# Performance work log

Measured on AMD Instinct MI355X. Metric: run time of the kernel, lower is better.

Reference implementation:

```python
import jax, jax.numpy as jnp
import numpy as np

FEAT = 1024
B = 1024
S = 64


def setup_inputs() -> dict:
    key = jax.random.key(0)
    ks = jax.random.split(key, 6)
    scale_ih = 1.0 / np.sqrt(2 * FEAT)
    scale_hh = 1.0 / np.sqrt(FEAT)
    return {
        "query": jax.random.normal(ks[0], (B, FEAT), jnp.float32) * 0.1,
        "support_context": jax.random.normal(ks[1], (S, FEAT), jnp.float32) * 0.1,
        "W_ih": jax.random.normal(ks[2], (4 * FEAT, 2 * FEAT), jnp.float32) * scale_ih,
        "W_hh": jax.random.normal(ks[3], (4 * FEAT, FEAT), jnp.float32) * scale_hh,
        "b_ih": jax.random.normal(ks[4], (4 * FEAT,), jnp.float32) * scale_hh,
        "b_hh": jax.random.normal(ks[5], (4 * FEAT,), jnp.float32) * scale_hh,
    }


def reference(query, support_context, W_ih, W_hh, b_ih, b_hh):
    # query: [B, F]; support_context: [S, F]; steps == S
    hidden = query
    cell = jnp.zeros_like(query)
    support_t = support_context.T  # [F, S]

    def step(carry, _):
        h, c = carry
        attn = jax.nn.softmax(h @ support_t, axis=1)          # [B, S]
        readout = attn @ support_context                      # [B, F]
        x = jnp.concatenate([query, readout], axis=1)         # [B, 2F]
        gates = x @ W_ih.T + b_ih + h @ W_hh.T + b_hh          # [B, 4F]
        i, f, g, o = jnp.split(gates, 4, axis=1)               # torch LSTMCell gate order
        c_new = jax.nn.sigmoid(f) * c + jax.nn.sigmoid(i) * jnp.tanh(g)
        h_new = jax.nn.sigmoid(o) * jnp.tanh(c_new) + query   # skip connection per original
        return (h_new, c_new), None

    (hidden, cell), _ = jax.lax.scan(step, (hidden, cell), None,
                                     length=support_context.shape[0])
    return hidden
```

## Files before the change

### kernel.cpp

```cpp
#include <hip/hip_runtime.h>
#include <hip/hip_bf16.h>


typedef __attribute__((ext_vector_type(8))) __bf16 bf16x8;
typedef __attribute__((ext_vector_type(4))) float f32x4;
typedef __attribute__((ext_vector_type(8))) unsigned short ushort8;

__device__ __forceinline__ ushort f2bf(float f) {
  union { float f; unsigned int u; } v; v.f = f;
  unsigned int u = v.u;
  u += 0x7FFFu + ((u >> 16) & 1u);
  return (ushort)(u >> 16);
}
__device__ __forceinline__ float bf2f(ushort u) {
  union { float f; unsigned int u; } v; v.u = ((unsigned int)u) << 16; return v.f;
}
__device__ __forceinline__ float sigm_(float x) { return 1.f / (1.f + __expf(-x)); }
__device__ __forceinline__ float tanh_(float x) {
  x = fminf(15.f, fmaxf(-15.f, x));
  float e = __expf(2.f * x);
  return (e - 1.f) / (e + 1.f);
}
__device__ __forceinline__ void async16(ushort* lds, const ushort* g) {
  __builtin_amdgcn_global_load_lds(
      (const __attribute__((address_space(1))) void*)g,
      (__attribute__((address_space(3))) void*)lds, 16, 0, 0);
}
__device__ __forceinline__ int permrow(int n) {
  int g = n >> 10, j = n & 1023;
  return ((j >> 4) << 6) | (g << 4) | (j & 15);
}

__global__ __launch_bounds__(256) void prep_kernel(
    const float* __restrict__ query, const float* __restrict__ support,
    const float* __restrict__ W_ih, const float* __restrict__ W_hh,
    const float* __restrict__ b_ih, const float* __restrict__ b_hh,
    ushort* __restrict__ Wq_bf, ushort* __restrict__ Wcomb,
    float* __restrict__ bias_p, ushort* __restrict__ X0,
    float* __restrict__ c, ushort* __restrict__ Wr_bf,
    ushort* __restrict__ Sb)
{
  int g = blockIdx.x * 256 + threadIdx.x;
  int n = g >> 10, k = g & 1023;
  int np = permrow(n);
  Wq_bf[(size_t)np * 1024 + k] = f2bf(W_ih[(size_t)n * 2048 + k]);
  Wr_bf[(size_t)n * 1024 + k]  = f2bf(W_ih[(size_t)n * 2048 + 1024 + k]);
  Wcomb[(size_t)np * 1088 + k] = f2bf(W_hh[(size_t)n * 1024 + k]);
  if (g < 1024 * 1024) {
    X0[g] = f2bf(query[g]);
    c[g] = 0.f;
  }
  if (g < 4096) bias_p[permrow(g)] = b_ih[g] + b_hh[g];
  if (g < 65536) Sb[g] = f2bf(support[g]);
}

__global__ __launch_bounds__(256) void sw_mfma(
    const ushort* __restrict__ Wr, const ushort* __restrict__ Sb,
    ushort* __restrict__ Wcomb)
{
  __shared__ ushort As[3][128 * 32];
  __shared__ ushort Bs[3][64 * 32];
  const int t = threadIdx.x;
  const int bm0 = blockIdx.x * 128;
  const int w = t >> 6, l = t & 63;
  const int wm = w * 32;
  const int srow = t >> 2, scol = (t & 3) * 8;
  const ushort* ga0 = Wr + (size_t)(bm0 + srow) * 1024 + scol;
  const ushort* ga1 = Wr + (size_t)(bm0 + 64 + srow) * 1024 + scol;
  const ushort* gb0 = Sb + (size_t)srow * 1024 + scol;
  const int fr = l & 15, fk = (l >> 4) * 8, fq = l >> 4;
  f32x4 acc[2][4] = {};
  const int nt = 32;
  async16(&As[0][t * 8], ga0); async16(&As[0][2048 + t * 8], ga1);
  async16(&Bs[0][t * 8], gb0);
  async16(&As[1][t * 8], ga0 + 32); async16(&As[1][2048 + t * 8], ga1 + 32);
  async16(&Bs[1][t * 8], gb0 + 32);
  for (int it = 0; it < nt; it++) {
    if (it + 1 < nt) { asm volatile("s_waitcnt vmcnt(3)" ::: "memory"); }
    else             { asm volatile("s_waitcnt vmcnt(0)" ::: "memory"); }
    __builtin_amdgcn_s_barrier();
    __builtin_amdgcn_sched_barrier(0);
    const int b = it % 3;
    const ushort* pa = &As[b][(wm + fr) * 32 + fk];
    const ushort* pb = &Bs[b][fr * 32 + fk];
    bf16x8 af[2], bfv[4];
#pragma unroll
    for (int mi = 0; mi < 2; mi++) af[mi] = *(const bf16x8*)(pa + mi * 512);
#pragma unroll
    for (int ni = 0; ni < 4; ni++) bfv[ni] = *(const bf16x8*)(pb + ni * 512);
    if (it + 2 < nt) {
      const int pbuf = (it + 2) % 3;
      const int k0 = (it + 2) << 5;
      async16(&As[pbuf][t * 8], ga0 + k0); async16(&As[pbuf][2048 + t * 8], ga1 + k0);
      async16(&Bs[pbuf][t * 8], gb0 + k0);
    }
#pragma unroll
    for (int mi = 0; mi < 2; mi++)
#pragma unroll
      for (int ni = 0; ni < 4; ni++)
        acc[mi][ni] = __builtin_amdgcn_mfma_f32_16x16x32_bf16(af[mi], bfv[ni], acc[mi][ni], 0, 0, 0);
  }
#pragma unroll
  for (int mi = 0; mi < 2; mi++)
#pragma unroll
    for (int ni = 0; ni < 4; ni++) {
      int s = ni * 16 + fr;
      int row0 = bm0 + wm + mi * 16 + fq * 4;
#pragma unroll
      for (int jj = 0; jj < 4; jj++)
        Wcomb[(size_t)permrow(row0 + jj) * 1088 + 1024 + s] = f2bf(acc[mi][ni][jj]);
    }
}

__global__ __launch_bounds__(256) void gemm_base(
    const ushort* __restrict__ A, const ushort* __restrict__ Bw,
    const float* __restrict__ bias, float* __restrict__ Cout)
{
  __shared__ ushort As[3][2][64 * 32];
  __shared__ ushort Bs[3][2][128 * 32];
  const int t = threadIdx.x;
  const int bid = blockIdx.x;
  const int xcd = bid & 7, idx = bid >> 3;
  const int bx = idx & 15, byy = idx >> 4;
  const int by = xcd * 4 + byy;
  const int m0 = bx * 64, n0 = by * 128;
  const int w = t >> 6, l = t & 63;
  const int wm = (w >> 1) * 32, wn = (w & 1) * 64;
  const int srow = t >> 2, scol = (t & 3) * 8;
  const ushort* ga  = A  + (size_t)(m0 + srow) * 1024 + scol;
  const ushort* gb0 = Bw + (size_t)(n0 + srow) * 1024 + scol;
  const ushort* gb1 = Bw + (size_t)(n0 + 64 + srow) * 1024 + scol;
  const int fr = l & 15, fk = (l >> 4) * 8, fq = l >> 4;
  f32x4 acc[2][4] = {};
  const int nt = 16;
#define BSTAGE(buf, k0)                                       \
  async16(&As[buf][0][t * 8], ga + (k0));                     \
  async16(&As[buf][1][t * 8], ga + (k0) + 32);                \
  async16(&Bs[buf][0][t * 8], gb0 + (k0));                    \
  async16(&Bs[buf][0][2048 + t * 8], gb1 + (k0));             \
  async16(&Bs[buf][1][t * 8], gb0 + (k0) + 32);               \
  async16(&Bs[buf][1][2048 + t * 8], gb1 + (k0) + 32);
  BSTAGE(0, 0)
  BSTAGE(1, 64)
  for (int it = 0; it < nt; it++) {
    if (it + 1 < nt) { asm volatile("s_waitcnt vmcnt(6)" ::: "memory"); }
    else             { asm volatile("s_waitcnt vmcnt(0)" ::: "memory"); }
    __builtin_amdgcn_s_barrier();
    __builtin_amdgcn_sched_barrier(0);
    if (it + 2 < nt) { const int pb = (it + 2) % 3; const int k0 = (it + 2) << 6; BSTAGE(pb, k0) }
    const int b = it % 3;
#pragma unroll
    for (int kk = 0; kk < 2; kk++) {
      const ushort* pa = &As[b][kk][(wm + fr) * 32 + fk];
      const ushort* pb2 = &Bs[b][kk][(wn + fr) * 32 + fk];
      bf16x8 af[2], bfv[4];
#pragma unroll
      for (int mi = 0; mi < 2; mi++) af[mi] = *(const bf16x8*)(pa + mi * 512);
#pragma unroll
      for (int ni = 0; ni < 4; ni++) bfv[ni] = *(const bf16x8*)(pb2 + ni * 512);
      __builtin_amdgcn_s_setprio(1);
#pragma unroll
      for (int mi = 0; mi < 2; mi++)
#pragma unroll
        for (int ni = 0; ni < 4; ni++)
          acc[mi][ni] = __builtin_amdgcn_mfma_f32_16x16x32_bf16(af[mi], bfv[ni], acc[mi][ni], 0, 0, 0);
      __builtin_amdgcn_s_setprio(0);
    }
  }
#undef BSTAGE
#pragma unroll
  for (int mi = 0; mi < 2; mi++)
#pragma unroll
    for (int ni = 0; ni < 4; ni++) {
      int col = n0 + wn + ni * 16 + fr;
      int row0 = m0 + wm + mi * 16 + fq * 4;
      float bv = bias[col];
#pragma unroll
      for (int jj = 0; jj < 4; jj++)
        Cout[(size_t)(row0 + jj) * 4096 + col] = acc[mi][ni][jj] + bv;
    }
}

__global__ __launch_bounds__(256, 2) void gemm_fused(
    const ushort* __restrict__ A,
    const ushort* __restrict__ Wcomb,
    const ushort* __restrict__ Sb,
    const float* __restrict__ base,
    float* __restrict__ cbuf, const float* __restrict__ query,
    ushort* __restrict__ Xout, float* __restrict__ outp)
{
  __shared__ ushort As[3][2][64 * 32];
  __shared__ ushort Bs[3][2][128 * 32];
  const int t = threadIdx.x;
  const int bid = blockIdx.x;
  const int xcd = bid & 7, idx = bid >> 3;
  const int bx = idx & 15, byy = idx >> 4;
  const int by = xcd * 4 + byy;
  const int m0 = bx * 64, n0 = by * 128;
  const int w = t >> 6, l = t & 63;
  const int wm = (w >> 1) * 32, wn = (w & 1) * 64;
  const int srow = t >> 2, scol = (t & 3) * 8;
  const ushort* ga  = A + (size_t)(m0 + srow) * 1024 + scol;
  const ushort* gb0 = Wcomb + (size_t)(n0 + srow) * 1088 + scol;
  const ushort* gb1 = Wcomb + (size_t)(n0 + 64 + srow) * 1088 + scol;
  const int fr = l & 15, fk = (l >> 4) * 8, fq = l >> 4;
  const ushort* gsb = Sb + (size_t)((w & 1) * 32 + fr) * 1024 + fk;
  f32x4 acc[2][4] = {};
  f32x4 lacc[2][2] = {};
#define FSTAGE_A(buf, k0)                                     \
  async16(&As[buf][0][t * 8], ga + (k0));                     \
  async16(&As[buf][1][t * 8], ga + (k0) + 32);
#define FSTAGE_B(buf, k0)                                     \
  async16(&Bs[buf][0][t * 8], gb0 + (k0));                    \
  async16(&Bs[buf][0][2048 + t * 8], gb1 + (k0));             \
  async16(&Bs[buf][1][t * 8], gb0 + (k0) + 32);               \
  async16(&Bs[buf][1][2048 + t * 8], gb1 + (k0) + 32);
  FSTAGE_A(0, 0) FSTAGE_B(0, 0)
  FSTAGE_A(1, 64) FSTAGE_B(1, 64)
  asm volatile("s_waitcnt vmcnt(6)" ::: "memory");
  for (int it = 0; it < 16; it++) {
    __builtin_amdgcn_s_barrier();
    __builtin_amdgcn_sched_barrier(0);
    const int k0 = it << 6;
    bf16x8 sb00 = *(const bf16x8*)(gsb + k0);
    bf16x8 sb01 = *(const bf16x8*)(gsb + k0 + 32);
    bf16x8 sb10 = *(const bf16x8*)(gsb + k0 + 16384);
    bf16x8 sb11 = *(const bf16x8*)(gsb + k0 + 16384 + 32);
    if (it <= 13) { const int pb = (it + 2) % 3; FSTAGE_A(pb, k0 + 128) FSTAGE_B(pb, k0 + 128) }
    else if (it == 14) { FSTAGE_B(1, 1024) }
    const int b = it % 3;
    bf16x8 af2[2][2];
#pragma unroll
    for (int kk = 0; kk < 2; kk++) {
      const ushort* pa = &As[b][kk][(wm + fr) * 32 + fk];
      const ushort* pb2 = &Bs[b][kk][(wn + fr) * 32 + fk];
      bf16x8 bfv[4];
#pragma unroll
      for (int mi = 0; mi < 2; mi++) af2[kk][mi] = *(const bf16x8*)(pa + mi * 512);
#pragma unroll
      for (int ni = 0; ni < 4; ni++) bfv[ni] = *(const bf16x8*)(pb2 + ni * 512);
      __builtin_amdgcn_s_setprio(1);
#pragma unroll
      for (int mi = 0; mi < 2; mi++)
#pragma unroll
        for (int ni = 0; ni < 4; ni++)
          acc[mi][ni] = __builtin_amdgcn_mfma_f32_16x16x32_bf16(af2[kk][mi], bfv[ni], acc[mi][ni], 0, 0, 0);
      __builtin_amdgcn_s_setprio(0);
    }
    if (it <= 13)      { asm volatile("s_waitcnt vmcnt(6)" ::: "memory"); }
    else if (it == 14) { asm volatile("s_waitcnt vmcnt(4)" ::: "memory"); }
    else               { asm volatile("s_waitcnt vmcnt(0)" ::: "memory"); }
    __builtin_amdgcn_sched_barrier(0);
    lacc[0][0] = __builtin_amdgcn_mfma_f32_16x16x32_bf16(af2[0][0], sb00, lacc[0][0], 0, 0, 0);
    lacc[0][1] = __builtin_amdgcn_mfma_f32_16x16x32_bf16(af2[0][0], sb10, lacc[0][1], 0, 0, 0);
    lacc[1][0] = __builtin_amdgcn_mfma_f32_16x16x32_bf16(af2[0][1], sb00, lacc[1][0], 0, 0, 0);
    lacc[1][1] = __builtin_amdgcn_mfma_f32_16x16x32_bf16(af2[0][1], sb10, lacc[1][1], 0, 0, 0);
    lacc[0][0] = __builtin_amdgcn_mfma_f32_16x16x32_bf16(af2[1][0], sb01, lacc[0][0], 0, 0, 0);
    lacc[0][1] = __builtin_amdgcn_mfma_f32_16x16x32_bf16(af2[1][0], sb11, lacc[0][1], 0, 0, 0);
    lacc[1][0] = __builtin_amdgcn_mfma_f32_16x16x32_bf16(af2[1][1], sb01, lacc[1][0], 0, 0, 0);
    lacc[1][1] = __builtin_amdgcn_mfma_f32_16x16x32_bf16(af2[1][1], sb11, lacc[1][1], 0, 0, 0);
  }
  __builtin_amdgcn_s_barrier();
  {
    float* lg = (float*)&Bs[0][0][0];
    const int sbase = (w & 1) * 32;
#pragma unroll
    for (int mi = 0; mi < 2; mi++)
#pragma unroll
      for (int ni = 0; ni < 2; ni++) {
        int s = sbase + ni * 16 + fr;
        int r0 = wm + mi * 16 + fq * 4;
#pragma unroll
        for (int jj = 0; jj < 4; jj++)
          lg[(r0 + jj) * 64 + s] = lacc[mi][ni][jj];
      }
  }
  __syncthreads();
  {
    const int r = t >> 2, q = t & 3;
    float* lg = (float*)&Bs[0][0][0];
    float p[16];
#pragma unroll
    for (int i = 0; i < 16; i++) p[i] = lg[r * 64 + q * 16 + i];
    float mx = p[0];
#pragma unroll
    for (int i = 1; i < 16; i++) mx = fmaxf(mx, p[i]);
    mx = fmaxf(mx, __shfl_xor(mx, 1));
    mx = fmaxf(mx, __shfl_xor(mx, 2));
    float sm = 0.f;
#pragma unroll
    for (int i = 0; i < 16; i++) { p[i] = __expf(p[i] - mx); sm += p[i]; }
    sm += __shfl_xor(sm, 1);
    sm += __shfl_xor(sm, 2);
    float inv = 1.f / sm;
    ushort* at = &As[1][q >> 1][r * 32 + (q & 1) * 16];
#pragma unroll
    for (int i = 0; i < 16; i++) at[i] = f2bf(p[i] * inv);
  }
  __syncthreads();
#pragma unroll
  for (int kk = 0; kk < 2; kk++) {
    const ushort* pa = &As[1][kk][(wm + fr) * 32 + fk];
    const ushort* pb2 = &Bs[1][kk][(wn + fr) * 32 + fk];
    bf16x8 af[2], bfv[4];
#pragma unroll
    for (int mi = 0; mi < 2; mi++) af[mi] = *(const bf16x8*)(pa + mi * 512);
#pragma unroll
    for (int ni = 0; ni < 4; ni++) bfv[ni] = *(const bf16x8*)(pb2 + ni * 512);
    __builtin_amdgcn_s_setprio(1);
#pragma unroll
    for (int mi = 0; mi < 2; mi++)
#pragma unroll
      for (int ni = 0; ni < 4; ni++)
        acc[mi][ni] = __builtin_amdgcn_mfma_f32_16x16x32_bf16(af[mi], bfv[ni], acc[mi][ni], 0, 0, 0);
    __builtin_amdgcn_s_setprio(0);
  }
#undef FSTAGE_A
#undef FSTAGE_B
  const int jcol = (((n0 + wn) >> 6) << 4) + fr;
#pragma unroll
  for (int mi = 0; mi < 2; mi++) {
#pragma unroll
    for (int jj = 0; jj < 4; jj++) {
      int row = m0 + wm + mi * 16 + fq * 4 + jj;
      const float* bp = base + (size_t)row * 4096 + (n0 + wn);
      float gi = acc[mi][0][jj] + bp[fr];
      float gf = acc[mi][1][jj] + bp[16 + fr];
      float gg = acc[mi][2][jj] + bp[32 + fr];
      float go = acc[mi][3][jj] + bp[48 + fr];
      size_t cidx = (size_t)row * 1024 + jcol;
      float cv = cbuf[cidx];
      float cn = sigm_(gf) * cv + sigm_(gi) * tanh_(gg);
      float hn = sigm_(go) * tanh_(cn) + query[cidx];
      cbuf[cidx] = cn;
      Xout[cidx] = f2bf(hn);
      if (outp) outp[cidx] = hn;
    }
  }
}

extern "C" void kernel_launch(void* const* d_in, const int* in_sizes, int n_in,
                              void* d_out, int out_size, void* d_ws, size_t ws_size,
                              hipStream_t stream) {
  const float* query   = (const float*)d_in[0];
  const float* support = (const float*)d_in[1];
  const float* W_ih    = (const float*)d_in[2];
  const float* W_hh    = (const float*)d_in[3];
  const float* b_ih    = (const float*)d_in[4];
  const float* b_hh    = (const float*)d_in[5];
  float* out = (float*)d_out;

  char* ws = (char*)d_ws;
  size_t off = 0;
  auto alloc = [&](size_t bytes) {
    void* p = ws + off;
    off += (bytes + 255) & ~(size_t)255;
    return p;
  };
  ushort* Wq_bf  = (ushort*)alloc((size_t)4096 * 1024 * 2);
  ushort* Wcomb  = (ushort*)alloc((size_t)4096 * 1088 * 2);
  ushort* Wr_bf  = (ushort*)alloc((size_t)4096 * 1024 * 2);
  ushort* Sb     = (ushort*)alloc((size_t)64 * 1024 * 2);
  float*  bias_p = (float*) alloc((size_t)4096 * 4);
  float*  base   = (float*) alloc((size_t)1024 * 4096 * 4);
  ushort* X0     = (ushort*)alloc((size_t)1024 * 1024 * 2);
  ushort* X1     = (ushort*)alloc((size_t)1024 * 1024 * 2);
  float*  c      = (float*) alloc((size_t)1024 * 1024 * 4);

  prep_kernel<<<16384, 256, 0, stream>>>(query, support, W_ih, W_hh, b_ih, b_hh,
                                         Wq_bf, Wcomb, bias_p, X0, c, Wr_bf, Sb);
  sw_mfma<<<32, 256, 0, stream>>>(Wr_bf, Sb, Wcomb);
  gemm_base<<<512, 256, 0, stream>>>(X0, Wq_bf, bias_p, base);
  for (int step = 0; step < 64; step++) {
    ushort* Xc = (step & 1) ? X1 : X0;
    ushort* Xn = (step & 1) ? X0 : X1;
    gemm_fused<<<512, 256, 0, stream>>>(Xc, Wcomb, Sb, base,
                                        c, query, Xn,
                                        (step == 63) ? out : nullptr);
  }
}
```

Baseline: 1.945 ms.

## Store base gates as packed bf16 and prefetch epilogue operands before softmax

```diff
diff --git a/kernel.cpp b/kernel.cpp
--- a/kernel.cpp
+++ b/kernel.cpp
@@ -4,7 +4,8 @@
 
 typedef __attribute__((ext_vector_type(8))) __bf16 bf16x8;
 typedef __attribute__((ext_vector_type(4))) float f32x4;
-typedef __attribute__((ext_vector_type(8))) unsigned short ushort8;
+
+#define MFMA __builtin_amdgcn_mfma_f32_16x16x32_bf16
 
 __device__ __forceinline__ ushort f2bf(float f) {
   union { float f; unsigned int u; } v; v.f = f;
@@ -98,7 +99,7 @@
     for (int mi = 0; mi < 2; mi++)
 #pragma unroll
       for (int ni = 0; ni < 4; ni++)
-        acc[mi][ni] = __builtin_amdgcn_mfma_f32_16x16x32_bf16(af[mi], bfv[ni], acc[mi][ni], 0, 0, 0);
+        acc[mi][ni] = MFMA(af[mi], bfv[ni], acc[mi][ni], 0, 0, 0);
   }
 #pragma unroll
   for (int mi = 0; mi < 2; mi++)
@@ -114,7 +115,7 @@
 
 __global__ __launch_bounds__(256) void gemm_base(
     const ushort* __restrict__ A, const ushort* __restrict__ Bw,
-    const float* __restrict__ bias, float* __restrict__ Cout)
+    const float* __restrict__ bias, ushort* __restrict__ basep)
 {
   __shared__ ushort As[3][2][64 * 32];
   __shared__ ushort Bs[3][2][128 * 32];
@@ -163,21 +164,23 @@
       for (int mi = 0; mi < 2; mi++)
 #pragma unroll
         for (int ni = 0; ni < 4; ni++)
-          acc[mi][ni] = __builtin_amdgcn_mfma_f32_16x16x32_bf16(af[mi], bfv[ni], acc[mi][ni], 0, 0, 0);
+          acc[mi][ni] = MFMA(af[mi], bfv[ni], acc[mi][ni], 0, 0, 0);
       __builtin_amdgcn_s_setprio(0);
     }
   }
 #undef BSTAGE
+  const int jcol = (((n0 + wn) >> 6) << 4) + fr;
 #pragma unroll
   for (int mi = 0; mi < 2; mi++)
 #pragma unroll
-    for (int ni = 0; ni < 4; ni++) {
-      int col = n0 + wn + ni * 16 + fr;
-      int row0 = m0 + wm + mi * 16 + fq * 4;
-      float bv = bias[col];
-#pragma unroll
-      for (int jj = 0; jj < 4; jj++)
-        Cout[(size_t)(row0 + jj) * 4096 + col] = acc[mi][ni][jj] + bv;
+    for (int jj = 0; jj < 4; jj++) {
+      int row = m0 + wm + mi * 16 + fq * 4 + jj;
+      ushort4 pk;
+      pk.x = f2bf(acc[mi][0][jj] + bias[n0 + wn + fr]);
+      pk.y = f2bf(acc[mi][1][jj] + bias[n0 + wn + 16 + fr]);
+      pk.z = f2bf(acc[mi][2][jj] + bias[n0 + wn + 32 + fr]);
+      pk.w = f2bf(acc[mi][3][jj] + bias[n0 + wn + 48 + fr]);
+      *(ushort4*)&basep[((size_t)row * 1024 + jcol) * 4] = pk;
     }
 }
 
@@ -185,7 +188,7 @@
     const ushort* __restrict__ A,
     const ushort* __restrict__ Wcomb,
     const ushort* __restrict__ Sb,
-    const float* __restrict__ base,
+    const ushort* __restrict__ basep,
     float* __restrict__ cbuf, const float* __restrict__ query,
     ushort* __restrict__ Xout, float* __restrict__ outp)
 {
@@ -244,25 +247,43 @@
       for (int mi = 0; mi < 2; mi++)
 #pragma unroll
         for (int ni = 0; ni < 4; ni++)
-          acc[mi][ni] = __builtin_amdgcn_mfma_f32_16x16x32_bf16(af2[kk][mi], bfv[ni], acc[mi][ni], 0, 0, 0);
+          acc[mi][ni] = MFMA(af2[kk][mi], bfv[ni], acc[mi][ni], 0, 0, 0);
       __builtin_amdgcn_s_setprio(0);
     }
     if (it <= 13)      { asm volatile("s_waitcnt vmcnt(6)" ::: "memory"); }
     else if (it == 14) { asm volatile("s_waitcnt vmcnt(4)" ::: "memory"); }
     else               { asm volatile("s_waitcnt vmcnt(0)" ::: "memory"); }
     __builtin_amdgcn_sched_barrier(0);
-    lacc[0][0] = __builtin_amdgcn_mfma_f32_16x16x32_bf16(af2[0][0], sb00, lacc[0][0], 0, 0, 0);
-    lacc[0][1] = __builtin_amdgcn_mfma_f32_16x16x32_bf16(af2[0][0], sb10, lacc[0][1], 0, 0, 0);
-    lacc[1][0] = __builtin_amdgcn_mfma_f32_16x16x32_bf16(af2[0][1], sb00, lacc[1][0], 0, 0, 0);
-    lacc[1][1] = __builtin_amdgcn_mfma_f32_16x16x32_bf16(af2[0][1], sb10, lacc[1][1], 0, 0, 0);
-    lacc[0][0] = __builtin_amdgcn_mfma_f32_16x16x32_bf16(af2[1][0], sb01, lacc[0][0], 0, 0, 0);
-    lacc[0][1] = __builtin_amdgcn_mfma_f32_16x16x32_bf16(af2[1][0], sb11, lacc[0][1], 0, 0, 0);
-    lacc[1][0] = __builtin_amdgcn_mfma_f32_16x16x32_bf16(af2[1][1], sb01, lacc[1][0], 0, 0, 0);
-    lacc[1][1] = __builtin_amdgcn_mfma_f32_16x16x32_bf16(af2[1][1], sb11, lacc[1][1], 0, 0, 0);
-  }
+    lacc[0][0] = MFMA(af2[0][0], sb00, lacc[0][0], 0, 0, 0);
+    lacc[0][1] = MFMA(af2[0][0], sb10, lacc[0][1], 0, 0, 0);
+    lacc[1][0] = MFMA(af2[0][1], sb00, lacc[1][0], 0, 0, 0);
+    lacc[1][1] = MFMA(af2[0][1], sb10, lacc[1][1], 0, 0, 0);
+    lacc[0][0] = MFMA(af2[1][0], sb01, lacc[0][0], 0, 0, 0);
+    lacc[0][1] = MFMA(af2[1][0], sb11, lacc[0][1], 0, 0, 0);
+    lacc[1][0] = MFMA(af2[1][1], sb01, lacc[1][0], 0, 0, 0);
+    lacc[1][1] = MFMA(af2[1][1], sb11, lacc[1][1], 0, 0, 0);
+  }
+#undef FSTAGE_A
+#undef FSTAGE_B
+  const int jcol = (((n0 + wn) >> 6) << 4) + fr;
+  ushort4 bpk[2][4];
+  float qv[2][4], cv[2][4];
+#pragma unroll
+  for (int mi = 0; mi < 2; mi++)
+#pragma unroll
+    for (int jj = 0; jj < 4; jj++) {
+      int row = m0 + wm + mi * 16 + fq * 4 + jj;
+      size_t cidx = (size_t)row * 1024 + jcol;
+      bpk[mi][jj] = *(const ushort4*)&basep[cidx * 4];
+      qv[mi][jj] = query[cidx];
+      cv[mi][jj] = cbuf[cidx];
+    }
+  asm volatile("s_waitcnt lgkmcnt(0)" ::: "memory");
   __builtin_amdgcn_s_barrier();
+  __builtin_amdgcn_sched_barrier(0);
   {
-    float* lg = (float*)&Bs[0][0][0];
+    float* lg = (float*)&Bs[1][0][0];
+    lg = (float*)&Bs[2][0][0];
     const int sbase = (w & 1) * 32;
 #pragma unroll
     for (int mi = 0; mi < 2; mi++)
@@ -275,10 +296,12 @@
           lg[(r0 + jj) * 64 + s] = lacc[mi][ni][jj];
       }
   }
-  __syncthreads();
+  asm volatile("s_waitcnt lgkmcnt(0)" ::: "memory");
+  __builtin_amdgcn_s_barrier();
+  __builtin_amdgcn_sched_barrier(0);
   {
     const int r = t >> 2, q = t & 3;
-    float* lg = (float*)&Bs[0][0][0];
+    float* lg = (float*)&Bs[2][0][0];
     float p[16];
 #pragma unroll
     for (int i = 0; i < 16; i++) p[i] = lg[r * 64 + q * 16 + i];
@@ -293,14 +316,16 @@
     sm += __shfl_xor(sm, 1);
     sm += __shfl_xor(sm, 2);
     float inv = 1.f / sm;
-    ushort* at = &As[1][q >> 1][r * 32 + (q & 1) * 16];
+    ushort* at = &As[2][q >> 1][r * 32 + (q & 1) * 16];
 #pragma unroll
     for (int i = 0; i < 16; i++) at[i] = f2bf(p[i] * inv);
   }
-  __syncthreads();
+  asm volatile("s_waitcnt lgkmcnt(0)" ::: "memory");
+  __builtin_amdgcn_s_barrier();
+  __builtin_amdgcn_sched_barrier(0);
 #pragma unroll
   for (int kk = 0; kk < 2; kk++) {
-    const ushort* pa = &As[1][kk][(wm + fr) * 32 + fk];
+    const ushort* pa = &As[2][kk][(wm + fr) * 32 + fk];
     const ushort* pb2 = &Bs[1][kk][(wn + fr) * 32 + fk];
     bf16x8 af[2], bfv[4];
 #pragma unroll
@@ -312,26 +337,22 @@
     for (int mi = 0; mi < 2; mi++)
 #pragma unroll
       for (int ni = 0; ni < 4; ni++)
-        acc[mi][ni] = __builtin_amdgcn_mfma_f32_16x16x32_bf16(af[mi], bfv[ni], acc[mi][ni], 0, 0, 0);
+        acc[mi][ni] = MFMA(af[mi], bfv[ni], acc[mi][ni], 0, 0, 0);
     __builtin_amdgcn_s_setprio(0);
   }
-#undef FSTAGE_A
-#undef FSTAGE_B
-  const int jcol = (((n0 + wn) >> 6) << 4) + fr;
 #pragma unroll
   for (int mi = 0; mi < 2; mi++) {
 #pragma unroll
     for (int jj = 0; jj < 4; jj++) {
       int row = m0 + wm + mi * 16 + fq * 4 + jj;
-      const float* bp = base + (size_t)row * 4096 + (n0 + wn);
-      float gi = acc[mi][0][jj] + bp[fr];
-      float gf = acc[mi][1][jj] + bp[16 + fr];
-      float gg = acc[mi][2][jj] + bp[32 + fr];
-      float go = acc[mi][3][jj] + bp[48 + fr];
       size_t cidx = (size_t)row * 1024 + jcol;
-      float cv = cbuf[cidx];
-      float cn = sigm_(gf) * cv + sigm_(gi) * tanh_(gg);
-      float hn = sigm_(go) * tanh_(cn) + query[cidx];
+      ushort4 pk = bpk[mi][jj];
+      float gi = acc[mi][0][jj] + bf2f(pk.x);
+      float gf = acc[mi][1][jj] + bf2f(pk.y);
+      float gg = acc[mi][2][jj] + bf2f(pk.z);
+      float go = acc[mi][3][jj] + bf2f(pk.w);
+      float cn = sigm_(gf) * cv[mi][jj] + sigm_(gi) * tanh_(gg);
+      float hn = sigm_(go) * tanh_(cn) + qv[mi][jj];
       cbuf[cidx] = cn;
       Xout[cidx] = f2bf(hn);
       if (outp) outp[cidx] = hn;
@@ -362,7 +383,7 @@
   ushort* Wr_bf  = (ushort*)alloc((size_t)4096 * 1024 * 2);
   ushort* Sb     = (ushort*)alloc((size_t)64 * 1024 * 2);
   float*  bias_p = (float*) alloc((size_t)4096 * 4);
-  float*  base   = (float*) alloc((size_t)1024 * 4096 * 4);
+  ushort* basep  = (ushort*)alloc((size_t)1024 * 4096 * 2);
   ushort* X0     = (ushort*)alloc((size_t)1024 * 1024 * 2);
   ushort* X1     = (ushort*)alloc((size_t)1024 * 1024 * 2);
   float*  c      = (float*) alloc((size_t)1024 * 1024 * 4);
@@ -370,11 +391,11 @@
   prep_kernel<<<16384, 256, 0, stream>>>(query, support, W_ih, W_hh, b_ih, b_hh,
                                          Wq_bf, Wcomb, bias_p, X0, c, Wr_bf, Sb);
   sw_mfma<<<32, 256, 0, stream>>>(Wr_bf, Sb, Wcomb);
-  gemm_base<<<512, 256, 0, stream>>>(X0, Wq_bf, bias_p, base);
+  gemm_base<<<512, 256, 0, stream>>>(X0, Wq_bf, bias_p, basep);
   for (int step = 0; step < 64; step++) {
     ushort* Xc = (step & 1) ? X1 : X0;
     ushort* Xn = (step & 1) ? X0 : X1;
-    gemm_fused<<<512, 256, 0, stream>>>(Xc, Wcomb, Sb, base,
+    gemm_fused<<<512, 256, 0, stream>>>(Xc, Wcomb, Sb, basep,
                                         c, query, Xn,
                                         (step == 63) ? out : nullptr);
   }
```

After: 1.838 ms. -5.5%, faster.
